# Kernel optimization log

Measured on AMD Instinct MI355X. Metric: run time of the kernel, lower is better.

## Reference

```python
import jax, jax.numpy as jnp
import numpy as np

NORM_EPS = 1e-6


def setup_inputs() -> dict:
    key = jax.random.key(0)
    k1, k2 = jax.random.split(key)
    in_features, out_features = 4096, 4096
    x = jax.random.normal(k1, (2, 2048, in_features), dtype=jnp.float32)
    scale = 1.0 / np.sqrt(in_features)
    weight = jax.random.normal(k2, (out_features, in_features), dtype=jnp.float32) * scale
    norm_weight = jnp.ones((in_features,), dtype=jnp.float32)
    return {"x": x, "weight": weight, "norm_weight": norm_weight}


def reference(x, weight, norm_weight):
    # RMSNorm over the last dim
    rms = jnp.sqrt(jnp.mean(x * x, axis=-1, keepdims=True) + NORM_EPS)
    x_n = x / rms * norm_weight
    # ternary weight quantization (absmean scale alpha)
    alpha = jnp.maximum(jnp.mean(jnp.abs(weight)), 1e-10)
    w_q = jnp.clip(jnp.round(weight / alpha), -1.0, 1.0)
    # per-token int8 activation quantization (absmax scale gamma)
    gamma = jnp.maximum(jnp.max(jnp.abs(x_n), axis=-1, keepdims=True), 1e-10)
    x_q = jnp.clip(jnp.round(x_n * 127.0 / gamma), -128.0, 127.0)
    # rescaled matmul: y = x_q @ w_q.T * (alpha * gamma / 127)
    y = jnp.einsum('bsk,nk->bsn', x_q, w_q) * (alpha * gamma / 127.0)
    return y
```

## Files before the change

### kernel.cpp

```cpp
#include <hip/hip_runtime.h>
#include <cstdint>
#include <cstddef>


#define KD 4096
#define MD 4096
#define ND 4096

typedef int i32x4 __attribute__((ext_vector_type(4)));

__device__ __forceinline__ void gl2lds16(const signed char* g, signed char* l) {
  __builtin_amdgcn_global_load_lds(
      (const __attribute__((address_space(1))) void*)g,
      (__attribute__((address_space(3))) void*)l, 16, 0, 0);
}

__device__ __forceinline__ float wave_sum(float v) {
#pragma unroll
  for (int off = 32; off; off >>= 1) v += __shfl_down(v, off, 64);
  return v;
}
__device__ __forceinline__ float wave_max(float v) {
#pragma unroll
  for (int off = 32; off; off >>= 1) v = fmaxf(v, __shfl_down(v, off, 64));
  return v;
}


__global__ __launch_bounds__(256) void k_alpha_part(const float* __restrict__ w,
                                                    float* __restrict__ part) {
  __shared__ float red[4];
  const int tid = threadIdx.x;
  const float4* w4 = (const float4*)(w + (size_t)blockIdx.x * 4096);
  float s = 0.f;
#pragma unroll
  for (int i = 0; i < 4; ++i) {
    float4 v = w4[i * 256 + tid];
    s += fabsf(v.x) + fabsf(v.y) + fabsf(v.z) + fabsf(v.w);
  }
  s = wave_sum(s);
  if ((tid & 63) == 0) red[tid >> 6] = s;
  __syncthreads();
  if (tid == 0) part[blockIdx.x] = (red[0] + red[1]) + (red[2] + red[3]);
}


__global__ __launch_bounds__(256) void k_quant_all(const float* __restrict__ w,
                                                   const float* __restrict__ x,
                                                   const float* __restrict__ nw,
                                                   const float* __restrict__ part,
                                                   signed char* __restrict__ wq,
                                                   signed char* __restrict__ xq,
                                                   float* __restrict__ gamma,
                                                   float* __restrict__ alpha_out) {
  const int tid = threadIdx.x;
  const int bid = blockIdx.x;
  __shared__ float red[4];
  __shared__ float red2[4];

  if (bid < 4096) {
    float s = 0.f;
#pragma unroll
    for (int i = 0; i < 16; ++i) s += part[i * 256 + tid];
    s = wave_sum(s);
    if ((tid & 63) == 0) red[tid >> 6] = s;
    __syncthreads();
    const float alpha =
        fmaxf(((red[0] + red[1]) + (red[2] + red[3])) * (1.0f / 16777216.0f),
              1e-10f);
    if (bid == 0 && tid == 0) alpha_out[0] = alpha;

    const float4* w4 = (const float4*)(w + (size_t)bid * 4096);
    uint32_t* wqi = (uint32_t*)(wq + (size_t)bid * 4096);
#pragma unroll
    for (int i = 0; i < 4; ++i) {
      const int f = i * 256 + tid;
      float4 v = w4[f];
      int q0 = (int)fminf(fmaxf(rintf(v.x / alpha), -1.f), 1.f);
      int q1 = (int)fminf(fmaxf(rintf(v.y / alpha), -1.f), 1.f);
      int q2 = (int)fminf(fmaxf(rintf(v.z / alpha), -1.f), 1.f);
      int q3 = (int)fminf(fmaxf(rintf(v.w / alpha), -1.f), 1.f);
      wqi[f] = (uint32_t)(q0 & 255) | ((uint32_t)(q1 & 255) << 8) |
               ((uint32_t)(q2 & 255) << 16) | ((uint32_t)(q3 & 255) << 24);
    }
  } else {
    const int row = bid - 4096;
    const float4* x4 = (const float4*)(x + (size_t)row * 4096);
    const float4* n4 = (const float4*)nw;
    float4 xv[4], nv[4];
    float ss = 0.f;
#pragma unroll
    for (int i = 0; i < 4; ++i) {
      xv[i] = x4[i * 256 + tid];
      nv[i] = n4[i * 256 + tid];
      ss += xv[i].x * xv[i].x + xv[i].y * xv[i].y + xv[i].z * xv[i].z +
            xv[i].w * xv[i].w;
    }
    ss = wave_sum(ss);
    if ((tid & 63) == 0) red[tid >> 6] = ss;
    __syncthreads();
    const float tot = (red[0] + red[1]) + (red[2] + red[3]);
    const float rms = sqrtf(tot * (1.0f / 4096.0f) + 1e-6f);

    float4 xn[4];
    float mx = 0.f;
#pragma unroll
    for (int i = 0; i < 4; ++i) {
      xn[i].x = xv[i].x / rms * nv[i].x;
      xn[i].y = xv[i].y / rms * nv[i].y;
      xn[i].z = xv[i].z / rms * nv[i].z;
      xn[i].w = xv[i].w / rms * nv[i].w;
      mx = fmaxf(mx, fmaxf(fmaxf(fabsf(xn[i].x), fabsf(xn[i].y)),
                           fmaxf(fabsf(xn[i].z), fabsf(xn[i].w))));
    }
    mx = wave_max(mx);
    if ((tid & 63) == 0) red2[tid >> 6] = mx;
    __syncthreads();
    const float g = fmaxf(
        fmaxf(fmaxf(red2[0], red2[1]), fmaxf(red2[2], red2[3])), 1e-10f);
    if (tid == 0) gamma[row] = g;

    uint32_t* xqi = (uint32_t*)(xq + (size_t)row * 4096);
#pragma unroll
    for (int i = 0; i < 4; ++i) {
      const int f = i * 256 + tid;
      int q0 = (int)fminf(fmaxf(rintf(xn[i].x * 127.0f / g), -128.f), 127.f);
      int q1 = (int)fminf(fmaxf(rintf(xn[i].y * 127.0f / g), -128.f), 127.f);
      int q2 = (int)fminf(fmaxf(rintf(xn[i].z * 127.0f / g), -128.f), 127.f);
      int q3 = (int)fminf(fmaxf(rintf(xn[i].w * 127.0f / g), -128.f), 127.f);
      xqi[f] = (uint32_t)(q0 & 255) | ((uint32_t)(q1 & 255) << 8) |
               ((uint32_t)(q2 & 255) << 16) | ((uint32_t)(q3 & 255) << 24);
    }
  }
}


__global__ __launch_bounds__(256) void k_gemm(const signed char* __restrict__ xq,
                                              const signed char* __restrict__ wq,
                                              const float* __restrict__ gamma,
                                              const float* __restrict__ alpha_p,
                                              float* __restrict__ out) {
  __shared__ __align__(16) signed char As[128 * 128];
  __shared__ __align__(16) signed char Bs[128 * 128];
  const int tid = threadIdx.x;
  const int lane = tid & 63;
  const int wave = tid >> 6;
  const int wm = (wave >> 1) * 64;
  const int wn = (wave & 1) * 64;
  const int quad = lane >> 4;
  const int l16 = lane & 15;
  const int bm = blockIdx.y * 128;
  const int bn = blockIdx.x * 128;

  const signed char* Ag = xq + (size_t)bm * KD;
  const signed char* Bg = wq + (size_t)bn * KD;

  const int lr = lane >> 3;
  const int sc = (lane & 7) ^ lr;
  const signed char* agp[4];
  const signed char* bgp[4];
  signed char* la[4];
  signed char* lb[4];
#pragma unroll
  for (int i = 0; i < 4; ++i) {
    const int R = i * 32 + wave * 8 + lr;
    agp[i] = Ag + (size_t)R * KD + sc * 16;
    bgp[i] = Bg + (size_t)R * KD + sc * 16;
    la[i] = &As[(i * 32 + wave * 8) * 128];
    lb[i] = &Bs[(i * 32 + wave * 8) * 128];
  }

  i32x4 acc[4][4];
#pragma unroll
  for (int i = 0; i < 4; ++i)
#pragma unroll
    for (int j = 0; j < 4; ++j) acc[i][j] = (i32x4){0, 0, 0, 0};

  const int swz = l16 & 7;

  for (int k0 = 0; k0 < KD; k0 += 128) {
    __syncthreads();
#pragma unroll
    for (int i = 0; i < 4; ++i) gl2lds16(agp[i] + k0, la[i]);
#pragma unroll
    for (int i = 0; i < 4; ++i) gl2lds16(bgp[i] + k0, lb[i]);
    __syncthreads();

#pragma unroll
    for (int ks = 0; ks < 2; ++ks) {
      const int pos = ((ks * 4 + quad) ^ swz) * 16;
      i32x4 af[4], bf[4];
#pragma unroll
      for (int mi = 0; mi < 4; ++mi)
        af[mi] = *(const i32x4*)&As[(wm + mi * 16 + l16) * 128 + pos];
#pragma unroll
      for (int ni = 0; ni < 4; ++ni)
        bf[ni] = *(const i32x4*)&Bs[(wn + ni * 16 + l16) * 128 + pos];
#pragma unroll
      for (int mi = 0; mi < 4; ++mi)
#pragma unroll
        for (int ni = 0; ni < 4; ++ni)
          acc[mi][ni] = __builtin_amdgcn_mfma_i32_16x16x64_i8(af[mi], bf[ni],
                                                              acc[mi][ni], 0, 0, 0);
    }
  }

  const float alpha = alpha_p[0];
#pragma unroll
  for (int mi = 0; mi < 4; ++mi) {
#pragma unroll
    for (int r = 0; r < 4; ++r) {
      const int m = bm + wm + mi * 16 + quad * 4 + r;
      const float s = (alpha * gamma[m]) / 127.0f;
#pragma unroll
      for (int ni = 0; ni < 4; ++ni) {
        const int n = bn + wn + ni * 16 + l16;
        out[(size_t)m * ND + n] = (float)acc[mi][ni][r] * s;
      }
    }
  }
}


extern "C" void kernel_launch(void* const* d_in, const int* in_sizes, int n_in,
                              void* d_out, int out_size, void* d_ws, size_t ws_size,
                              hipStream_t stream) {
  const float* x = (const float*)d_in[0];
  const float* w = (const float*)d_in[1];
  const float* nw = (const float*)d_in[2];
  float* out = (float*)d_out;

  char* ws = (char*)d_ws;
  signed char* xq = (signed char*)ws;
  signed char* wq = (signed char*)(ws + ((size_t)1 << 24));
  float* gamma = (float*)(ws + ((size_t)2 << 24));
  float* part = (float*)(ws + ((size_t)2 << 24) + 16384);
  float* alpha = (float*)(ws + ((size_t)2 << 24) + 32768);

  k_alpha_part<<<4096, 256, 0, stream>>>(w, part);
  k_quant_all<<<8192, 256, 0, stream>>>(w, x, nw, part, wq, xq, gamma, alpha);
  dim3 g(ND / 128, MD / 128);
  k_gemm<<<g, 256, 0, stream>>>(xq, wq, gamma, alpha, out);
}
```

Measured before the change: 244.1 us.

## Fuse alpha reduction, quantization and GEMM into one cooperative persistent kernel

Merges the three kernels into one cooperative kernel that uses grid-wide syncs between the alpha partial sums, the activation quantization, the weight quantization and the GEMM phase. Blocks loop over rows and output tiles in a persistent style, with the grid size taken from occupancy and capped at the 1024 tiles. The aim is to remove kernel launch gaps and tail effects. In exchange it pays for two grid barriers and reads the weights twice, and the GEMM gets at most 1024 resident blocks with no extra scheduling flexibility.

```diff
diff --git a/kernel.cpp b/kernel.cpp
--- a/kernel.cpp
+++ b/kernel.cpp
@@ -1,11 +1,15 @@
 #include <hip/hip_runtime.h>
+#include <hip/hip_cooperative_groups.h>
 #include <cstdint>
 #include <cstddef>
+
+namespace cg = cooperative_groups;
 
 
 #define KD 4096
 #define MD 4096
 #define ND 4096
+#define NTILE 1024
 
 typedef int i32x4 __attribute__((ext_vector_type(4)));
 
@@ -26,52 +30,103 @@
   return v;
 }
 
-
-__global__ __launch_bounds__(256) void k_alpha_part(const float* __restrict__ w,
-                                                    float* __restrict__ part) {
+__global__ __launch_bounds__(256, 4) void k_fused(
+    const float* __restrict__ x, const float* __restrict__ w,
+    const float* __restrict__ nw, signed char* __restrict__ xq,
+    signed char* __restrict__ wq, float* __restrict__ gamma,
+    float* __restrict__ part, float* __restrict__ out) {
+  __shared__ __align__(16) signed char As[128 * 128];
+  __shared__ __align__(16) signed char Bs[128 * 128];
   __shared__ float red[4];
+  __shared__ float red2[4];
+
   const int tid = threadIdx.x;
-  const float4* w4 = (const float4*)(w + (size_t)blockIdx.x * 4096);
+  const int bid = blockIdx.x;
+  const int nblk = gridDim.x;
+  cg::grid_group grid = cg::this_grid();
+
+  for (int row = bid; row < 4096; row += nblk) {
+    const float4* w4 = (const float4*)(w + (size_t)row * 4096);
+    float s = 0.f;
+#pragma unroll
+    for (int j = 0; j < 4; ++j) {
+      float4 v = w4[j * 256 + tid];
+      s += fabsf(v.x) + fabsf(v.y) + fabsf(v.z) + fabsf(v.w);
+    }
+    s = wave_sum(s);
+    __syncthreads();
+    if ((tid & 63) == 0) red[tid >> 6] = s;
+    __syncthreads();
+    if (tid == 0) part[row] = (red[0] + red[1]) + (red[2] + red[3]);
+  }
+
+  for (int row = bid; row < 4096; row += nblk) {
+    const float4* x4 = (const float4*)(x + (size_t)row * 4096);
+    const float4* n4 = (const float4*)nw;
+    float4 xv[4], nv[4];
+    float ss = 0.f;
+#pragma unroll
+    for (int i = 0; i < 4; ++i) {
+      xv[i] = x4[i * 256 + tid];
+      nv[i] = n4[i * 256 + tid];
+      ss += xv[i].x * xv[i].x + xv[i].y * xv[i].y + xv[i].z * xv[i].z +
+            xv[i].w * xv[i].w;
+    }
+    ss = wave_sum(ss);
+    __syncthreads();
+    if ((tid & 63) == 0) red[tid >> 6] = ss;
+    __syncthreads();
+    const float tot = (red[0] + red[1]) + (red[2] + red[3]);
+    const float rms = sqrtf(tot * (1.0f / 4096.0f) + 1e-6f);
+
+    float4 xn[4];
+    float mx = 0.f;
+#pragma unroll
+    for (int i = 0; i < 4; ++i) {
+      xn[i].x = xv[i].x / rms * nv[i].x;
+      xn[i].y = xv[i].y / rms * nv[i].y;
+      xn[i].z = xv[i].z / rms * nv[i].z;
+      xn[i].w = xv[i].w / rms * nv[i].w;
+      mx = fmaxf(mx, fmaxf(fmaxf(fabsf(xn[i].x), fabsf(xn[i].y)),
+                           fmaxf(fabsf(xn[i].z), fabsf(xn[i].w))));
+    }
+    mx = wave_max(mx);
+    __syncthreads();
+    if ((tid & 63) == 0) red2[tid >> 6] = mx;
+    __syncthreads();
+    const float g = fmaxf(
+        fmaxf(fmaxf(red2[0], red2[1]), fmaxf(red2[2], red2[3])), 1e-10f);
+    if (tid == 0) gamma[row] = g;
+
+    uint32_t* xqi = (uint32_t*)(xq + (size_t)row * 4096);
+#pragma unroll
+    for (int i = 0; i < 4; ++i) {
+      const int f = i * 256 + tid;
+      int q0 = (int)fminf(fmaxf(rintf(xn[i].x * 127.0f / g), -128.f), 127.f);
+      int q1 = (int)fminf(fmaxf(rintf(xn[i].y * 127.0f / g), -128.f), 127.f);
+      int q2 = (int)fminf(fmaxf(rintf(xn[i].z * 127.0f / g), -128.f), 127.f);
+      int q3 = (int)fminf(fmaxf(rintf(xn[i].w * 127.0f / g), -128.f), 127.f);
+      xqi[f] = (uint32_t)(q0 & 255) | ((uint32_t)(q1 & 255) << 8) |
+               ((uint32_t)(q2 & 255) << 16) | ((uint32_t)(q3 & 255) << 24);
+    }
+  }
+
+  grid.sync();
+
   float s = 0.f;
 #pragma unroll
-  for (int i = 0; i < 4; ++i) {
-    float4 v = w4[i * 256 + tid];
-    s += fabsf(v.x) + fabsf(v.y) + fabsf(v.z) + fabsf(v.w);
-  }
+  for (int i = 0; i < 16; ++i) s += part[i * 256 + tid];
   s = wave_sum(s);
+  __syncthreads();
   if ((tid & 63) == 0) red[tid >> 6] = s;
   __syncthreads();
-  if (tid == 0) part[blockIdx.x] = (red[0] + red[1]) + (red[2] + red[3]);
-}
-
-
-__global__ __launch_bounds__(256) void k_quant_all(const float* __restrict__ w,
-                                                   const float* __restrict__ x,
-                                                   const float* __restrict__ nw,
-                                                   const float* __restrict__ part,
-                                                   signed char* __restrict__ wq,
-                                                   signed char* __restrict__ xq,
-                                                   float* __restrict__ gamma,
-                                                   float* __restrict__ alpha_out) {
-  const int tid = threadIdx.x;
-  const int bid = blockIdx.x;
-  __shared__ float red[4];
-  __shared__ float red2[4];
-
-  if (bid < 4096) {
-    float s = 0.f;
-#pragma unroll
-    for (int i = 0; i < 16; ++i) s += part[i * 256 + tid];
-    s = wave_sum(s);
-    if ((tid & 63) == 0) red[tid >> 6] = s;
-    __syncthreads();
-    const float alpha =
-        fmaxf(((red[0] + red[1]) + (red[2] + red[3])) * (1.0f / 16777216.0f),
-              1e-10f);
-    if (bid == 0 && tid == 0) alpha_out[0] = alpha;
-
-    const float4* w4 = (const float4*)(w + (size_t)bid * 4096);
-    uint32_t* wqi = (uint32_t*)(wq + (size_t)bid * 4096);
+  const float alpha =
+      fmaxf(((red[0] + red[1]) + (red[2] + red[3])) * (1.0f / 16777216.0f),
+            1e-10f);
+
+  for (int row = bid; row < 4096; row += nblk) {
+    const float4* w4 = (const float4*)(w + (size_t)row * 4096);
+    uint32_t* wqi = (uint32_t*)(wq + (size_t)row * 4096);
 #pragma unroll
     for (int i = 0; i < 4; ++i) {
       const int f = i * 256 + tid;
@@ -83,139 +138,83 @@
       wqi[f] = (uint32_t)(q0 & 255) | ((uint32_t)(q1 & 255) << 8) |
                ((uint32_t)(q2 & 255) << 16) | ((uint32_t)(q3 & 255) << 24);
     }
-  } else {
-    const int row = bid - 4096;
-    const float4* x4 = (const float4*)(x + (size_t)row * 4096);
-    const float4* n4 = (const float4*)nw;
-    float4 xv[4], nv[4];
-    float ss = 0.f;
-#pragma unroll
-    for (int i = 0; i < 4; ++i) {
-      xv[i] = x4[i * 256 + tid];
-      nv[i] = n4[i * 256 + tid];
-      ss += xv[i].x * xv[i].x + xv[i].y * xv[i].y + xv[i].z * xv[i].z +
-            xv[i].w * xv[i].w;
-    }
-    ss = wave_sum(ss);
-    if ((tid & 63) == 0) red[tid >> 6] = ss;
-    __syncthreads();
-    const float tot = (red[0] + red[1]) + (red[2] + red[3]);
-    const float rms = sqrtf(tot * (1.0f / 4096.0f) + 1e-6f);
-
-    float4 xn[4];
-    float mx = 0.f;
-#pragma unroll
-    for (int i = 0; i < 4; ++i) {
-      xn[i].x = xv[i].x / rms * nv[i].x;
-      xn[i].y = xv[i].y / rms * nv[i].y;
-      xn[i].z = xv[i].z / rms * nv[i].z;
-      xn[i].w = xv[i].w / rms * nv[i].w;
-      mx = fmaxf(mx, fmaxf(fmaxf(fabsf(xn[i].x), fabsf(xn[i].y)),
-                           fmaxf(fabsf(xn[i].z), fabsf(xn[i].w))));
-    }
-    mx = wave_max(mx);
-    if ((tid & 63) == 0) red2[tid >> 6] = mx;
-    __syncthreads();
-    const float g = fmaxf(
-        fmaxf(fmaxf(red2[0], red2[1]), fmaxf(red2[2], red2[3])), 1e-10f);
-    if (tid == 0) gamma[row] = g;
-
-    uint32_t* xqi = (uint32_t*)(xq + (size_t)row * 4096);
-#pragma unroll
-    for (int i = 0; i < 4; ++i) {
-      const int f = i * 256 + tid;
-      int q0 = (int)fminf(fmaxf(rintf(xn[i].x * 127.0f / g), -128.f), 127.f);
-      int q1 = (int)fminf(fmaxf(rintf(xn[i].y * 127.0f / g), -128.f), 127.f);
-      int q2 = (int)fminf(fmaxf(rintf(xn[i].z * 127.0f / g), -128.f), 127.f);
-      int q3 = (int)fminf(fmaxf(rintf(xn[i].w * 127.0f / g), -128.f), 127.f);
-      xqi[f] = (uint32_t)(q0 & 255) | ((uint32_t)(q1 & 255) << 8) |
-               ((uint32_t)(q2 & 255) << 16) | ((uint32_t)(q3 & 255) << 24);
-    }
-  }
-}
-
-
-__global__ __launch_bounds__(256) void k_gemm(const signed char* __restrict__ xq,
-                                              const signed char* __restrict__ wq,
-                                              const float* __restrict__ gamma,
-                                              const float* __restrict__ alpha_p,
-                                              float* __restrict__ out) {
-  __shared__ __align__(16) signed char As[128 * 128];
-  __shared__ __align__(16) signed char Bs[128 * 128];
-  const int tid = threadIdx.x;
+  }
+
+  grid.sync();
+
   const int lane = tid & 63;
   const int wave = tid >> 6;
   const int wm = (wave >> 1) * 64;
   const int wn = (wave & 1) * 64;
   const int quad = lane >> 4;
   const int l16 = lane & 15;
-  const int bm = blockIdx.y * 128;
-  const int bn = blockIdx.x * 128;
-
-  const signed char* Ag = xq + (size_t)bm * KD;
-  const signed char* Bg = wq + (size_t)bn * KD;
-
   const int lr = lane >> 3;
   const int sc = (lane & 7) ^ lr;
-  const signed char* agp[4];
-  const signed char* bgp[4];
-  signed char* la[4];
-  signed char* lb[4];
-#pragma unroll
-  for (int i = 0; i < 4; ++i) {
-    const int R = i * 32 + wave * 8 + lr;
-    agp[i] = Ag + (size_t)R * KD + sc * 16;
-    bgp[i] = Bg + (size_t)R * KD + sc * 16;
-    la[i] = &As[(i * 32 + wave * 8) * 128];
-    lb[i] = &Bs[(i * 32 + wave * 8) * 128];
-  }
-
-  i32x4 acc[4][4];
-#pragma unroll
-  for (int i = 0; i < 4; ++i)
-#pragma unroll
-    for (int j = 0; j < 4; ++j) acc[i][j] = (i32x4){0, 0, 0, 0};
-
   const int swz = l16 & 7;
 
-  for (int k0 = 0; k0 < KD; k0 += 128) {
-    __syncthreads();
-#pragma unroll
-    for (int i = 0; i < 4; ++i) gl2lds16(agp[i] + k0, la[i]);
-#pragma unroll
-    for (int i = 0; i < 4; ++i) gl2lds16(bgp[i] + k0, lb[i]);
-    __syncthreads();
-
-#pragma unroll
-    for (int ks = 0; ks < 2; ++ks) {
-      const int pos = ((ks * 4 + quad) ^ swz) * 16;
-      i32x4 af[4], bf[4];
-#pragma unroll
-      for (int mi = 0; mi < 4; ++mi)
-        af[mi] = *(const i32x4*)&As[(wm + mi * 16 + l16) * 128 + pos];
-#pragma unroll
-      for (int ni = 0; ni < 4; ++ni)
-        bf[ni] = *(const i32x4*)&Bs[(wn + ni * 16 + l16) * 128 + pos];
-#pragma unroll
-      for (int mi = 0; mi < 4; ++mi)
+  for (int tile = bid; tile < NTILE; tile += nblk) {
+    const int bm = (tile >> 5) * 128;
+    const int bn = (tile & 31) * 128;
+    const signed char* Ag = xq + (size_t)bm * KD;
+    const signed char* Bg = wq + (size_t)bn * KD;
+
+    const signed char* agp[4];
+    const signed char* bgp[4];
+    signed char* la[4];
+    signed char* lb[4];
+#pragma unroll
+    for (int i = 0; i < 4; ++i) {
+      const int R = i * 32 + wave * 8 + lr;
+      agp[i] = Ag + (size_t)R * KD + sc * 16;
+      bgp[i] = Bg + (size_t)R * KD + sc * 16;
+      la[i] = &As[(i * 32 + wave * 8) * 128];
+      lb[i] = &Bs[(i * 32 + wave * 8) * 128];
+    }
+
+    i32x4 acc[4][4];
+#pragma unroll
+    for (int i = 0; i < 4; ++i)
+#pragma unroll
+      for (int j = 0; j < 4; ++j) acc[i][j] = (i32x4){0, 0, 0, 0};
+
+    for (int k0 = 0; k0 < KD; k0 += 128) {
+      __syncthreads();
+#pragma unroll
+      for (int i = 0; i < 4; ++i) gl2lds16(agp[i] + k0, la[i]);
+#pragma unroll
+      for (int i = 0; i < 4; ++i) gl2lds16(bgp[i] + k0, lb[i]);
+      __syncthreads();
+
+#pragma unroll
+      for (int ks = 0; ks < 2; ++ks) {
+        const int pos = ((ks * 4 + quad) ^ swz) * 16;
+        i32x4 af[4], bf[4];
+#pragma unroll
+        for (int mi = 0; mi < 4; ++mi)
+          af[mi] = *(const i32x4*)&As[(wm + mi * 16 + l16) * 128 + pos];
 #pragma unroll
         for (int ni = 0; ni < 4; ++ni)
-          acc[mi][ni] = __builtin_amdgcn_mfma_i32_16x16x64_i8(af[mi], bf[ni],
-                                                              acc[mi][ni], 0, 0, 0);
-    }
-  }
-
-  const float alpha = alpha_p[0];
-#pragma unroll
-  for (int mi = 0; mi < 4; ++mi) {
-#pragma unroll
-    for (int r = 0; r < 4; ++r) {
-      const int m = bm + wm + mi * 16 + quad * 4 + r;
-      const float s = (alpha * gamma[m]) / 127.0f;
-#pragma unroll
-      for (int ni = 0; ni < 4; ++ni) {
-        const int n = bn + wn + ni * 16 + l16;
-        out[(size_t)m * ND + n] = (float)acc[mi][ni][r] * s;
+          bf[ni] = *(const i32x4*)&Bs[(wn + ni * 16 + l16) * 128 + pos];
+#pragma unroll
+        for (int mi = 0; mi < 4; ++mi)
+#pragma unroll
+          for (int ni = 0; ni < 4; ++ni)
+            acc[mi][ni] = __builtin_amdgcn_mfma_i32_16x16x64_i8(
+                af[mi], bf[ni], acc[mi][ni], 0, 0, 0);
+      }
+    }
+
+#pragma unroll
+    for (int mi = 0; mi < 4; ++mi) {
+#pragma unroll
+      for (int r = 0; r < 4; ++r) {
+        const int m = bm + wm + mi * 16 + quad * 4 + r;
+        const float sc2 = (alpha * gamma[m]) / 127.0f;
+#pragma unroll
+        for (int ni = 0; ni < 4; ++ni) {
+          const int n = bn + wn + ni * 16 + l16;
+          out[(size_t)m * ND + n] = (float)acc[mi][ni][r] * sc2;
+        }
       }
     }
   }
@@ -235,10 +234,16 @@
   signed char* wq = (signed char*)(ws + ((size_t)1 << 24));
   float* gamma = (float*)(ws + ((size_t)2 << 24));
   float* part = (float*)(ws + ((size_t)2 << 24) + 16384);
-  float* alpha = (float*)(ws + ((size_t)2 << 24) + 32768);
-
-  k_alpha_part<<<4096, 256, 0, stream>>>(w, part);
-  k_quant_all<<<8192, 256, 0, stream>>>(w, x, nw, part, wq, xq, gamma, alpha);
-  dim3 g(ND / 128, MD / 128);
-  k_gemm<<<g, 256, 0, stream>>>(xq, wq, gamma, alpha, out);
-}
+
+  int blocks_per_cu = 0;
+  (void)hipOccupancyMaxActiveBlocksPerMultiprocessor(
+      &blocks_per_cu, (const void*)k_fused, 256, 0);
+  if (blocks_per_cu < 1) blocks_per_cu = 1;
+  int nblk = blocks_per_cu * 256;
+  if (nblk > NTILE) nblk = NTILE;
+
+  void* args[] = {(void*)&x,  (void*)&w,     (void*)&nw,   (void*)&xq,
+                  (void*)&wq, (void*)&gamma, (void*)&part, (void*)&out};
+  hipLaunchCooperativeKernel((const void*)k_fused, dim3(nblk), dim3(256), args,
+                             0, stream);
+}
```

Result: slower. 449.5 us (+84.2%).
